# Performance work log

Hardware: AMD Instinct MI355X
Metric: run time of the kernel (lower is better)

## Reference

```python
import jax, jax.numpy as jnp
import numpy as np

META_HIDDEN = 32


def _meta_apply(t, mw1, mb1, mw2, mb2):
    # t: [..., 3] triples; meta MLP 3 -> META_HIDDEN -> 1 (ReLU)
    h = jax.nn.relu(jnp.einsum('...k,hk->...h', t, mw1) + mb1)
    return jnp.einsum('...h,h->...', h, mw2[0]) + mb2[0]


def _meta_update_layer(v_in, w, v_out, mw1, mb1, mw2, mb2):
    # v_in: [I] (batch-0 input activations), w: [O, I], v_out: [O] (batch-0 output activations)
    # Builds the triples [v_i, w_ij, v_j] for every (i, j) pair and runs one batched meta pass.
    t = jnp.stack([
        jnp.broadcast_to(v_in[None, :], w.shape),
        w,
        jnp.broadcast_to(v_out[:, None], w.shape),
    ], axis=-1)  # [O, I, 3]
    return _meta_apply(t, mw1, mb1, mw2, mb2)  # [O, I] new weights


def setup_inputs() -> dict:
    key = jax.random.key(0)
    ks = jax.random.split(key, 12)
    I, H1, H2, O, B = 1024, 2048, 2048, 1024, 32
    def lin(kw, fan_in, fan_out):
        s = 1.0 / np.sqrt(fan_in)
        return jax.random.uniform(kw, (fan_out, fan_in), jnp.float32, -s, s)
    x = jax.random.normal(ks[0], (B, I), jnp.float32)
    w1 = lin(ks[1], I, H1); b1 = jax.random.uniform(ks[2], (H1,), jnp.float32, -1/np.sqrt(I), 1/np.sqrt(I))
    w2 = lin(ks[3], H1, H2); b2 = jax.random.uniform(ks[4], (H2,), jnp.float32, -1/np.sqrt(H1), 1/np.sqrt(H1))
    w3 = lin(ks[5], H2, O); b3 = jax.random.uniform(ks[6], (O,), jnp.float32, -1/np.sqrt(H2), 1/np.sqrt(H2))
    # meta network 3 -> META_HIDDEN -> 1
    mw1 = lin(ks[7], 3, META_HIDDEN); mb1 = jax.random.uniform(ks[8], (META_HIDDEN,), jnp.float32, -1/np.sqrt(3), 1/np.sqrt(3))
    mw2 = lin(ks[9], META_HIDDEN, 1); mb2 = jax.random.uniform(ks[10], (1,), jnp.float32, -1/np.sqrt(META_HIDDEN), 1/np.sqrt(META_HIDDEN))
    return {"x": x, "w1": w1, "b1": b1, "w2": w2, "b2": b2, "w3": w3, "b3": b3,
            "mw1": mw1, "mb1": mb1, "mw2": mw2, "mb2": mb2}


def reference(x, w1, b1, w2, b2, w3, b3, mw1, mb1, mw2, mb2):
    # Main 3-layer MLP forward (ReLU after every layer, including the last, as in the source).
    a0 = x
    a1 = jax.nn.relu(a0 @ w1.T + b1)
    a2 = jax.nn.relu(a1 @ w2.T + b2)
    out = jax.nn.relu(a2 @ w3.T + b3)
    # Per-weight meta update: original code loops over every (input, output) neuron pair of
    # each fc weight and writes meta_weight([v_i, w_ij, v_j]) back into the weight.
    # Only batch row 0 of the activations is used (impulse[i].data[0, idx]).
    nw1 = _meta_update_layer(a0[0], w1, a1[0], mw1, mb1, mw2, mb2)
    nw2 = _meta_update_layer(a1[0], w2, a2[0], mw1, mb1, mw2, mb2)
    nw3 = _meta_update_layer(a2[0], w3, out[0], mw1, mb1, mw2, mb2)
    return out, nw1, nw2, nw3
```

## Files before the change

kernel.cpp:

```cpp
#include <hip/hip_runtime.h>

#define THREADS 256

typedef float f2 __attribute__((ext_vector_type(2)));

__global__ __launch_bounds__(THREADS) void fwd_partial(
    const float* __restrict__ A, const float* __restrict__ W,
    float* __restrict__ P, int K, int O, int KL) {
  __shared__ float Wt[64][64];
  __shared__ float At[32][64];
  const int tid = threadIdx.x;
  const int obase = blockIdx.x * 64;
  const int ks = blockIdx.y;
  const int kbeg = ks * KL;
  const int kend = kbeg + KL;
  const int to = tid & 31;
  const int tb = tid >> 5;

  float acc[2][4] = {{0.f,0.f,0.f,0.f},{0.f,0.f,0.f,0.f}};

  for (int k0 = kbeg; k0 < kend; k0 += 64) {
    #pragma unroll
    for (int t = 0; t < 4; ++t) {
      const int id4 = tid + t * THREADS;
      const int r  = id4 >> 4;
      const int c4 = id4 & 15;
      const float4 v = *reinterpret_cast<const float4*>(
          &W[(size_t)(obase + r) * K + k0 + (c4 << 2)]);
      *reinterpret_cast<float4*>(&Wt[r][(c4 ^ (r & 15)) << 2]) = v;
    }
    #pragma unroll
    for (int t = 0; t < 2; ++t) {
      const int id4 = tid + t * THREADS;
      const int r  = id4 >> 4;
      const int c4 = id4 & 15;
      const float4 v = *reinterpret_cast<const float4*>(
          &A[(size_t)r * K + k0 + (c4 << 2)]);
      *reinterpret_cast<float4*>(&At[r][c4 << 2]) = v;
    }
    __syncthreads();

    #pragma unroll
    for (int kk = 0; kk < 64; kk += 4) {
      float4 wv[2], av[4];
      const int g = (((kk >> 2) ^ (to & 15)) << 2);
      wv[0] = *reinterpret_cast<const float4*>(&Wt[to][g]);
      wv[1] = *reinterpret_cast<const float4*>(&Wt[to + 32][g]);
      #pragma unroll
      for (int j = 0; j < 4; ++j)
        av[j] = *reinterpret_cast<const float4*>(&At[(tb << 2) + j][kk]);
      #pragma unroll
      for (int i = 0; i < 2; ++i) {
        #pragma unroll
        for (int j = 0; j < 4; ++j) {
          acc[i][j] = fmaf(wv[i].x, av[j].x, acc[i][j]);
          acc[i][j] = fmaf(wv[i].y, av[j].y, acc[i][j]);
          acc[i][j] = fmaf(wv[i].z, av[j].z, acc[i][j]);
          acc[i][j] = fmaf(wv[i].w, av[j].w, acc[i][j]);
        }
      }
    }
    __syncthreads();
  }

  #pragma unroll
  for (int i = 0; i < 2; ++i) {
    #pragma unroll
    for (int j = 0; j < 4; ++j) {
      const int b = (tb << 2) + j;
      const int o = obase + to + 32 * i;
      P[((size_t)ks * 32 + b) * O + o] = acc[i][j];
    }
  }
}

template<int KS, int O_SH>
__global__ __launch_bounds__(THREADS) void fwd_reduce_t(
    const float* __restrict__ P, const float* __restrict__ bias,
    float* __restrict__ C) {
  const int idx = blockIdx.x * THREADS + threadIdx.x;
  const int b = idx >> O_SH;
  const int o = idx & ((1 << O_SH) - 1);
  float s = 0.f;
  #pragma unroll
  for (int ks = 0; ks < KS; ++ks)
    s += P[((size_t)(ks * 32 + b) << O_SH) + o];
  C[idx] = fmaxf(s + bias[o], 0.f);
}

__global__ __launch_bounds__(THREADS) void meta_all(
    const float* __restrict__ w1, const float* __restrict__ w2, const float* __restrict__ w3,
    const float* __restrict__ a0, const float* __restrict__ a1, const float* __restrict__ a2,
    const float* __restrict__ a3,
    float* __restrict__ n1, float* __restrict__ n2, float* __restrict__ n3,
    const float* __restrict__ mw1, const float* __restrict__ mb1,
    const float* __restrict__ mw2, const float* __restrict__ mb2) {
  const int g = blockIdx.x * THREADS + threadIdx.x;
  const int n1c = (2048 * 1024) / 8;
  const int n2c = (2048 * 2048) / 8;

  const float* W; const float* vin; const float* vout; float* nw;
  int sh, e;
  if (g < n1c)            { W = w1; vin = a0; vout = a1; nw = n1; sh = 10; e = g; }
  else if (g < n1c + n2c) { W = w2; vin = a1; vout = a2; nw = n2; sh = 11; e = g - n1c; }
  else                    { W = w3; vin = a2; vout = a3; nw = n3; sh = 11; e = g - n1c - n2c; }

  const int base = e << 3;
  const int o = base >> sh;
  const int i0 = base & ((1 << sh) - 1);

  f2 wv[4], vv[4];
  {
    float4 t0 = *reinterpret_cast<const float4*>(&W[base]);
    float4 t1 = *reinterpret_cast<const float4*>(&W[base + 4]);
    wv[0] = (f2){t0.x, t0.y}; wv[1] = (f2){t0.z, t0.w};
    wv[2] = (f2){t1.x, t1.y}; wv[3] = (f2){t1.z, t1.w};
    float4 u0 = *reinterpret_cast<const float4*>(&vin[i0]);
    float4 u1 = *reinterpret_cast<const float4*>(&vin[i0 + 4]);
    vv[0] = (f2){u0.x, u0.y}; vv[1] = (f2){u0.z, u0.w};
    vv[2] = (f2){u1.x, u1.y}; vv[3] = (f2){u1.z, u1.w};
  }
  const float vo = vout[o];
  const float c2 = mb2[0];

  float r[32];
  #pragma unroll
  for (int j = 0; j < 32; ++j)
    r[j] = fmaf(mw1[3 * j + 2], vo, mb1[j]);

  f2 acc[4];
  #pragma unroll
  for (int p = 0; p < 4; ++p) acc[p] = (f2){c2, c2};

  const f2 zero = (f2){0.f, 0.f};
  #pragma unroll
  for (int j = 0; j < 32; ++j) {
    const float aj = mw1[3 * j];
    const float bj = mw1[3 * j + 1];
    const float mj = mw2[j];
    const f2 a2v = (f2){aj, aj};
    const f2 b2v = (f2){bj, bj};
    const f2 m2v = (f2){mj, mj};
    const f2 r2v = (f2){r[j], r[j]};
    #pragma unroll
    for (int p = 0; p < 4; ++p) {
#if __has_builtin(__builtin_elementwise_fma) && __has_builtin(__builtin_elementwise_max)
      f2 q = __builtin_elementwise_fma(a2v, vv[p], r2v);
      f2 h = __builtin_elementwise_fma(b2v, wv[p], q);
      h = __builtin_elementwise_max(h, zero);
      acc[p] = __builtin_elementwise_fma(m2v, h, acc[p]);
#else
      f2 h;
      h.x = fmaxf(fmaf(bj, wv[p].x, fmaf(aj, vv[p].x, r[j])), 0.f);
      h.y = fmaxf(fmaf(bj, wv[p].y, fmaf(aj, vv[p].y, r[j])), 0.f);
      acc[p].x = fmaf(mj, h.x, acc[p].x);
      acc[p].y = fmaf(mj, h.y, acc[p].y);
#endif
    }
  }

  float4 o0 = make_float4(acc[0].x, acc[0].y, acc[1].x, acc[1].y);
  float4 o1 = make_float4(acc[2].x, acc[2].y, acc[3].x, acc[3].y);
  *reinterpret_cast<float4*>(&nw[base])     = o0;
  *reinterpret_cast<float4*>(&nw[base + 4]) = o1;
}

extern "C" void kernel_launch(void* const* d_in, const int* in_sizes, int n_in,
                              void* d_out, int out_size, void* d_ws, size_t ws_size,
                              hipStream_t stream) {
  const float* x   = (const float*)d_in[0];
  const float* w1  = (const float*)d_in[1];
  const float* b1  = (const float*)d_in[2];
  const float* w2  = (const float*)d_in[3];
  const float* b2  = (const float*)d_in[4];
  const float* w3  = (const float*)d_in[5];
  const float* b3  = (const float*)d_in[6];
  const float* mw1 = (const float*)d_in[7];
  const float* mb1 = (const float*)d_in[8];
  const float* mw2 = (const float*)d_in[9];
  const float* mb2 = (const float*)d_in[10];

  float* out = (float*)d_out;
  float* n1  = out + 32 * 1024;
  float* n2  = n1 + 2048 * 1024;
  float* n3  = n2 + 2048 * 2048;

  float* ws   = (float*)d_ws;
  float* a1   = ws;
  float* a2   = ws + 65536;
  float* part = ws + 131072;

  fwd_partial<<<dim3(2048 / 64, 16), THREADS, 0, stream>>>(x, w1, part, 1024, 2048, 64);
  fwd_reduce_t<16, 11><<<(32 * 2048) / THREADS, THREADS, 0, stream>>>(part, b1, a1);
  fwd_partial<<<dim3(2048 / 64, 32), THREADS, 0, stream>>>(a1, w2, part, 2048, 2048, 64);
  fwd_reduce_t<32, 11><<<(32 * 2048) / THREADS, THREADS, 0, stream>>>(part, b2, a2);
  fwd_partial<<<dim3(1024 / 64, 32), THREADS, 0, stream>>>(a2, w3, part, 2048, 1024, 64);
  fwd_reduce_t<32, 10><<<(32 * 1024) / THREADS, THREADS, 0, stream>>>(part, b3, out);

  meta_all<<<4096, THREADS, 0, stream>>>(w1, w2, w3, x, a1, a2, out,
                                         n1, n2, n3, mw1, mb1, mw2, mb2);
}
```

Baseline: 60.77 us.

## Fuse meta-update blocks into forward GEMM launches to overlap independent work

Measured after the change: 59.89 us. About the same (-1.4%).

```diff
diff --git a/kernel.cpp b/kernel.cpp
--- a/kernel.cpp
+++ b/kernel.cpp
@@ -1,101 +1,17 @@
 #include <hip/hip_runtime.h>
 
-#define THREADS 256
+#define NT 256
 
 typedef float f2 __attribute__((ext_vector_type(2)));
 
-__global__ __launch_bounds__(THREADS) void fwd_partial(
-    const float* __restrict__ A, const float* __restrict__ W,
-    float* __restrict__ P, int K, int O, int KL) {
-  __shared__ float Wt[64][64];
-  __shared__ float At[32][64];
-  const int tid = threadIdx.x;
-  const int obase = blockIdx.x * 64;
-  const int ks = blockIdx.y;
-  const int kbeg = ks * KL;
-  const int kend = kbeg + KL;
-  const int to = tid & 31;
-  const int tb = tid >> 5;
-
-  float acc[2][4] = {{0.f,0.f,0.f,0.f},{0.f,0.f,0.f,0.f}};
-
-  for (int k0 = kbeg; k0 < kend; k0 += 64) {
-    #pragma unroll
-    for (int t = 0; t < 4; ++t) {
-      const int id4 = tid + t * THREADS;
-      const int r  = id4 >> 4;
-      const int c4 = id4 & 15;
-      const float4 v = *reinterpret_cast<const float4*>(
-          &W[(size_t)(obase + r) * K + k0 + (c4 << 2)]);
-      *reinterpret_cast<float4*>(&Wt[r][(c4 ^ (r & 15)) << 2]) = v;
-    }
-    #pragma unroll
-    for (int t = 0; t < 2; ++t) {
-      const int id4 = tid + t * THREADS;
-      const int r  = id4 >> 4;
-      const int c4 = id4 & 15;
-      const float4 v = *reinterpret_cast<const float4*>(
-          &A[(size_t)r * K + k0 + (c4 << 2)]);
-      *reinterpret_cast<float4*>(&At[r][c4 << 2]) = v;
-    }
-    __syncthreads();
-
-    #pragma unroll
-    for (int kk = 0; kk < 64; kk += 4) {
-      float4 wv[2], av[4];
-      const int g = (((kk >> 2) ^ (to & 15)) << 2);
-      wv[0] = *reinterpret_cast<const float4*>(&Wt[to][g]);
-      wv[1] = *reinterpret_cast<const float4*>(&Wt[to + 32][g]);
-      #pragma unroll
-      for (int j = 0; j < 4; ++j)
-        av[j] = *reinterpret_cast<const float4*>(&At[(tb << 2) + j][kk]);
-      #pragma unroll
-      for (int i = 0; i < 2; ++i) {
-        #pragma unroll
-        for (int j = 0; j < 4; ++j) {
-          acc[i][j] = fmaf(wv[i].x, av[j].x, acc[i][j]);
-          acc[i][j] = fmaf(wv[i].y, av[j].y, acc[i][j]);
-          acc[i][j] = fmaf(wv[i].z, av[j].z, acc[i][j]);
-          acc[i][j] = fmaf(wv[i].w, av[j].w, acc[i][j]);
-        }
-      }
-    }
-    __syncthreads();
-  }
-
-  #pragma unroll
-  for (int i = 0; i < 2; ++i) {
-    #pragma unroll
-    for (int j = 0; j < 4; ++j) {
-      const int b = (tb << 2) + j;
-      const int o = obase + to + 32 * i;
-      P[((size_t)ks * 32 + b) * O + o] = acc[i][j];
-    }
-  }
-}
-
-template<int KS, int O_SH>
-__global__ __launch_bounds__(THREADS) void fwd_reduce_t(
-    const float* __restrict__ P, const float* __restrict__ bias,
-    float* __restrict__ C) {
-  const int idx = blockIdx.x * THREADS + threadIdx.x;
-  const int b = idx >> O_SH;
-  const int o = idx & ((1 << O_SH) - 1);
-  float s = 0.f;
-  #pragma unroll
-  for (int ks = 0; ks < KS; ++ks)
-    s += P[((size_t)(ks * 32 + b) << O_SH) + o];
-  C[idx] = fmaxf(s + bias[o], 0.f);
-}
-
-__global__ __launch_bounds__(THREADS) void meta_all(
+__device__ __forceinline__ void meta_body(
+    int g,
     const float* __restrict__ w1, const float* __restrict__ w2, const float* __restrict__ w3,
     const float* __restrict__ a0, const float* __restrict__ a1, const float* __restrict__ a2,
     const float* __restrict__ a3,
     float* __restrict__ n1, float* __restrict__ n2, float* __restrict__ n3,
     const float* __restrict__ mw1, const float* __restrict__ mb1,
     const float* __restrict__ mw2, const float* __restrict__ mb2) {
-  const int g = blockIdx.x * THREADS + threadIdx.x;
   const int n1c = (2048 * 1024) / 8;
   const int n2c = (2048 * 2048) / 8;
 
@@ -165,6 +81,122 @@
   *reinterpret_cast<float4*>(&nw[base + 4]) = o1;
 }
 
+template<int KL>
+__device__ __forceinline__ void gemm_body(
+    int gbid, const float* __restrict__ A, const float* __restrict__ W,
+    float* __restrict__ P, int K, int O,
+    float* __restrict__ Wt, float* __restrict__ At) {
+  constexpr int NG = KL / 4;
+  constexpr int PM = NG - 1;
+  const int tid = threadIdx.x;
+  const int ks = gbid & 31;
+  const int obase = (gbid >> 5) << 7;
+  const int kbeg = ks * KL;
+
+  #pragma unroll
+  for (int t = 0; t < (128 * NG) / NT; ++t) {
+    const int s = tid + t * NT;
+    const int r = s / NG, p = s % NG;
+    const float4 v = *reinterpret_cast<const float4*>(
+        &W[(size_t)(obase + r) * K + kbeg + 4 * p]);
+    *reinterpret_cast<float4*>(&Wt[r * KL + 4 * (p ^ (r & PM))]) = v;
+  }
+  #pragma unroll
+  for (int t = 0; t < (32 * NG + NT - 1) / NT; ++t) {
+    const int s = tid + t * NT;
+    if ((32 * NG) % NT == 0 || s < 32 * NG) {
+      const int r = s / NG, p = s % NG;
+      *reinterpret_cast<float4*>(&At[r * KL + 4 * p]) =
+          *reinterpret_cast<const float4*>(&A[(size_t)r * K + kbeg + 4 * p]);
+    }
+  }
+  __syncthreads();
+
+  const int to = tid & 31;
+  const int b0 = (tid >> 5) << 2;
+  float acc[4][4];
+  #pragma unroll
+  for (int i = 0; i < 4; ++i)
+    #pragma unroll
+    for (int j = 0; j < 4; ++j) acc[i][j] = 0.f;
+
+  #pragma unroll
+  for (int gq = 0; gq < NG; ++gq) {
+    float4 av[4], wv[4];
+    #pragma unroll
+    for (int j = 0; j < 4; ++j)
+      av[j] = *reinterpret_cast<const float4*>(&At[(b0 + j) * KL + 4 * gq]);
+    const int c = 4 * (gq ^ (to & PM));
+    #pragma unroll
+    for (int i = 0; i < 4; ++i)
+      wv[i] = *reinterpret_cast<const float4*>(&Wt[(to + 32 * i) * KL + c]);
+    #pragma unroll
+    for (int i = 0; i < 4; ++i) {
+      #pragma unroll
+      for (int j = 0; j < 4; ++j) {
+        acc[i][j] = fmaf(wv[i].x, av[j].x, acc[i][j]);
+        acc[i][j] = fmaf(wv[i].y, av[j].y, acc[i][j]);
+        acc[i][j] = fmaf(wv[i].z, av[j].z, acc[i][j]);
+        acc[i][j] = fmaf(wv[i].w, av[j].w, acc[i][j]);
+      }
+    }
+  }
+
+  #pragma unroll
+  for (int i = 0; i < 4; ++i)
+    #pragma unroll
+    for (int j = 0; j < 4; ++j)
+      P[(size_t)(ks * 32 + b0 + j) * O + obase + to + 32 * i] = acc[i][j];
+}
+
+template<int KL>
+__global__ __launch_bounds__(NT) void combo(
+    int nGemm,
+    const float* __restrict__ A, const float* __restrict__ W,
+    float* __restrict__ P, int K, int O,
+    int gbase,
+    const float* __restrict__ w1, const float* __restrict__ w2, const float* __restrict__ w3,
+    const float* __restrict__ a0, const float* __restrict__ a1, const float* __restrict__ a2,
+    const float* __restrict__ a3,
+    float* __restrict__ n1, float* __restrict__ n2, float* __restrict__ n3,
+    const float* __restrict__ mw1, const float* __restrict__ mb1,
+    const float* __restrict__ mw2, const float* __restrict__ mb2) {
+  __shared__ float Wt[128 * KL];
+  __shared__ float At[32 * KL];
+  const int bid = blockIdx.x;
+  if (bid < nGemm) {
+    gemm_body<KL>(bid, A, W, P, K, O, Wt, At);
+  } else {
+    const int g = gbase + (bid - nGemm) * NT + threadIdx.x;
+    meta_body(g, w1, w2, w3, a0, a1, a2, a3, n1, n2, n3, mw1, mb1, mw2, mb2);
+  }
+}
+
+__global__ __launch_bounds__(NT) void meta_only(
+    int gbase,
+    const float* __restrict__ w1, const float* __restrict__ w2, const float* __restrict__ w3,
+    const float* __restrict__ a0, const float* __restrict__ a1, const float* __restrict__ a2,
+    const float* __restrict__ a3,
+    float* __restrict__ n1, float* __restrict__ n2, float* __restrict__ n3,
+    const float* __restrict__ mw1, const float* __restrict__ mb1,
+    const float* __restrict__ mw2, const float* __restrict__ mb2) {
+  const int g = gbase + blockIdx.x * NT + threadIdx.x;
+  meta_body(g, w1, w2, w3, a0, a1, a2, a3, n1, n2, n3, mw1, mb1, mw2, mb2);
+}
+
+template<int OSH>
+__global__ __launch_bounds__(NT) void red32(
+    const float* __restrict__ P, const float* __restrict__ bias,
+    float* __restrict__ C) {
+  const int e = blockIdx.x * NT + threadIdx.x;
+  const int o = e & ((1 << OSH) - 1);
+  float s = 0.f;
+  #pragma unroll
+  for (int ks = 0; ks < 32; ++ks)
+    s += P[((size_t)ks << (5 + OSH)) + e];
+  C[e] = fmaxf(s + bias[o], 0.f);
+}
+
 extern "C" void kernel_launch(void* const* d_in, const int* in_sizes, int n_in,
                               void* d_out, int out_size, void* d_ws, size_t ws_size,
                               hipStream_t stream) {
@@ -185,18 +217,20 @@
   float* n2  = n1 + 2048 * 1024;
   float* n3  = n2 + 2048 * 2048;
 
-  float* ws   = (float*)d_ws;
-  float* a1   = ws;
-  float* a2   = ws + 65536;
-  float* part = ws + 131072;
-
-  fwd_partial<<<dim3(2048 / 64, 16), THREADS, 0, stream>>>(x, w1, part, 1024, 2048, 64);
-  fwd_reduce_t<16, 11><<<(32 * 2048) / THREADS, THREADS, 0, stream>>>(part, b1, a1);
-  fwd_partial<<<dim3(2048 / 64, 32), THREADS, 0, stream>>>(a1, w2, part, 2048, 2048, 64);
-  fwd_reduce_t<32, 11><<<(32 * 2048) / THREADS, THREADS, 0, stream>>>(part, b2, a2);
-  fwd_partial<<<dim3(1024 / 64, 32), THREADS, 0, stream>>>(a2, w3, part, 2048, 1024, 64);
-  fwd_reduce_t<32, 10><<<(32 * 1024) / THREADS, THREADS, 0, stream>>>(part, b3, out);
-
-  meta_all<<<4096, THREADS, 0, stream>>>(w1, w2, w3, x, a1, a2, out,
-                                         n1, n2, n3, mw1, mb1, mw2, mb2);
-}
+  float* ws = (float*)d_ws;
+  float* a1 = ws;
+  float* a2 = ws + 65536;
+  float* P  = ws + 131072;
+
+  combo<32><<<512, NT, 0, stream>>>(512, x, w1, P, 1024, 2048,
+      0, w1, w2, w3, x, a1, a2, out, n1, n2, n3, mw1, mb1, mw2, mb2);
+  red32<11><<<(32 * 2048) / NT, NT, 0, stream>>>(P, b1, a1);
+  combo<64><<<512 + 1024, NT, 0, stream>>>(512, a1, w2, P, 2048, 2048,
+      0, w1, w2, w3, x, a1, a2, out, n1, n2, n3, mw1, mb1, mw2, mb2);
+  red32<11><<<(32 * 2048) / NT, NT, 0, stream>>>(P, b2, a2);
+  combo<64><<<256 + 2048, NT, 0, stream>>>(256, a2, w3, P, 2048, 1024,
+      262144, w1, w2, w3, x, a1, a2, out, n1, n2, n3, mw1, mb1, mw2, mb2);
+  red32<10><<<(32 * 1024) / NT, NT, 0, stream>>>(P, b3, out);
+  meta_only<<<1024, NT, 0, stream>>>(786432, w1, w2, w3, x, a1, a2, out,
+                                     n1, n2, n3, mw1, mb1, mw2, mb2);
+}
```
